# Optimization experiments

Measured on AMD Instinct MI355X. Metric: run time of the kernel, lower is better.

The kernel has to match this reference:

```python
import jax, jax.numpy as jnp
import numpy as np

N_U, N_M, E, L = 100000, 20000, 2000000, 500000
F_U, F_M, H = 64, 128, 128


def setup_inputs() -> dict:
    key = jax.random.key(0)
    ks = jax.random.split(key, 48)
    p = lambda k, shape: jax.random.normal(k, shape, jnp.float32) * 0.02
    inp = {
        'x_user': jax.random.normal(ks[0], (N_U, F_U), jnp.float32),
        'x_movie': jax.random.normal(ks[1], (N_M, F_M), jnp.float32),
        'edge_index': jnp.stack([jax.random.randint(ks[2], (E,), 0, N_U),
                                 jax.random.randint(ks[3], (E,), 0, N_M)]),
        'edge_label_index': jnp.stack([jax.random.randint(ks[4], (L,), 0, N_U),
                                       jax.random.randint(ks[5], (L,), 0, N_M)]),
        # per-type input projections (LazyLinear)
        'lin_u_W': p(ks[6], (H, F_U)), 'lin_u_b': p(ks[7], (H,)),
        'lin_m_W': p(ks[8], (H, F_M)), 'lin_m_b': p(ks[9], (H,)),
        # BatchNorm (eval mode: running stats)
        'bn_u_g': 1.0 + p(ks[10], (H,)), 'bn_u_b': p(ks[11], (H,)),
        'bn_u_m': p(ks[12], (H,)) * 5.0,
        'bn_u_v': jax.random.uniform(ks[13], (H,), jnp.float32, 0.5, 1.5),
        'bn_m_g': 1.0 + p(ks[14], (H,)), 'bn_m_b': p(ks[15], (H,)),
        'bn_m_m': p(ks[16], (H,)) * 5.0,
        'bn_m_v': jax.random.uniform(ks[17], (H,), jnp.float32, 0.5, 1.5),
        # conv1: SAGEConv per relation (Wl applied to aggregated, Wr to root)
        'c1_um_Wl': p(ks[18], (H, H)), 'c1_um_bl': p(ks[19], (H,)), 'c1_um_Wr': p(ks[20], (H, H)),
        'c1_mu_Wl': p(ks[21], (H, H)), 'c1_mu_bl': p(ks[22], (H,)), 'c1_mu_Wr': p(ks[23], (H, H)),
        # conv2
        'c2_um_Wl': p(ks[24], (H, H)), 'c2_um_bl': p(ks[25], (H,)), 'c2_um_Wr': p(ks[26], (H, H)),
        'c2_mu_Wl': p(ks[27], (H, H)), 'c2_mu_bl': p(ks[28], (H,)), 'c2_mu_Wr': p(ks[29], (H, H)),
        # edge decoder MLP: 2H -> 4H -> 2H -> 1
        'dec_W1': p(ks[30], (4 * H, 2 * H)), 'dec_b1': p(ks[31], (4 * H,)),
        'dec_W2': p(ks[32], (2 * H, 4 * H)), 'dec_b2': p(ks[33], (2 * H,)),
        'dec_W3': p(ks[34], (1, 2 * H)), 'dec_b3': p(ks[35], (1,)),
    }
    return inp


def _bn(x, g, b, m, v):
    return (x - m) * jax.lax.rsqrt(v + 1e-5) * g + b


def _seg_mean(msg, dst, n):
    s = jax.ops.segment_sum(msg, dst, num_segments=n)
    c = jax.ops.segment_sum(jnp.ones((dst.shape[0], 1), msg.dtype), dst, num_segments=n)
    return s / jnp.maximum(c, 1.0)


def _sage(x_src, x_dst, src, dst, Wl, bl, Wr):
    # PyG SAGEConv(aggr='mean'): lin_l(mean of source msgs) + lin_r(x_dst)
    agg = _seg_mean(x_src[src], dst, x_dst.shape[0])
    return agg @ Wl.T + bl + x_dst @ Wr.T


def reference(x_user, x_movie, edge_index, edge_label_index,
              lin_u_W, lin_u_b, lin_m_W, lin_m_b,
              bn_u_g, bn_u_b, bn_u_m, bn_u_v,
              bn_m_g, bn_m_b, bn_m_m, bn_m_v,
              c1_um_Wl, c1_um_bl, c1_um_Wr, c1_mu_Wl, c1_mu_bl, c1_mu_Wr,
              c2_um_Wl, c2_um_bl, c2_um_Wr, c2_mu_Wl, c2_mu_bl, c2_mu_Wr,
              dec_W1, dec_b1, dec_W2, dec_b2, dec_W3, dec_b3):
    u, m = edge_index[0], edge_index[1]
    # per-type projection + BN(eval) + ReLU (Dropout is identity in eval)
    xu = jnp.maximum(_bn(x_user @ lin_u_W.T + lin_u_b, bn_u_g, bn_u_b, bn_u_m, bn_u_v), 0.0)
    xm = jnp.maximum(_bn(x_movie @ lin_m_W.T + lin_m_b, bn_m_g, bn_m_b, bn_m_m, bn_m_v), 0.0)
    # conv1: user->movie and movie->user (HeteroConv mean over 1 relation each)
    xm1 = jnp.maximum(_sage(xu, xm, u, m, c1_um_Wl, c1_um_bl, c1_um_Wr), 0.0)
    xu1 = jnp.maximum(_sage(xm, xu, m, u, c1_mu_Wl, c1_mu_bl, c1_mu_Wr), 0.0)
    # conv2 (no activation after, matches forward)
    zm = _sage(xu1, xm1, u, m, c2_um_Wl, c2_um_bl, c2_um_Wr)
    zu = _sage(xm1, xu1, m, u, c2_mu_Wl, c2_mu_bl, c2_mu_Wr)
    # edge decoder: gather + MLP
    feat = jnp.concatenate([zu[edge_label_index[0]], zm[edge_label_index[1]]], axis=-1)
    h = jnp.maximum(feat @ dec_W1.T + dec_b1, 0.0)
    h = jnp.maximum(h @ dec_W2.T + dec_b2, 0.0)
    return (h @ dec_W3.T + dec_b3)[:, 0]
```

## Files before the change

### kernel.cpp

```cpp
#include <hip/hip_runtime.h>

#define NU 100000
#define NM 20000
#define NE 2000000
#define NL 500000
#define H  128
#define MROW 48

typedef __attribute__((ext_vector_type(8))) short bf16x8;
typedef __attribute__((ext_vector_type(4))) float floatx4;
typedef __attribute__((ext_vector_type(8))) unsigned short u16x8;
typedef __attribute__((ext_vector_type(4))) unsigned short u16x4;

__device__ __forceinline__ unsigned short f2b(float x) {
    union { __bf16 h; unsigned short u; } v;
    v.h = (__bf16)x;
    return v.u;
}
__device__ __forceinline__ float b2f(unsigned short h) {
    union { unsigned u; float f; } v; v.u = ((unsigned)h) << 16;
    return v.f;
}

#define SFCH(r, c)  ((r) * 32 + (((c) + (r)) & 31))
#define SH1CH(r, c) ((r) * 16 + (((c) + (r)) & 15))
#define SH2CH(r, c) ((r) * 64 + (((c) + (r)) & 63))

struct PrepArgs {
    const float* luW; float* wtu;
    const float* lmW; float* wtm;
    const float* W1; const float* W2;
    unsigned short* W1p; unsigned short* W2p;
    const float* sw[8]; unsigned short* wsg;
    const int* ei; int* rp_m; int* rp_u; int* pos_m; int* pos_u;
};

__global__ __launch_bounds__(256) void prep1(PrepArgs a) {
    const int b = blockIdx.x, tid = threadIdx.x;
    if (b < 64) {
        const int n = H * 64;
        for (int i = b * 256 + tid; i < n; i += 64 * 256) {
            int r = i >> 6, c = i & 63;
            a.wtu[c * H + r] = a.luW[i];
        }
    } else if (b < 128) {
        const int n = H * H;
        for (int i = (b - 64) * 256 + tid; i < n; i += 64 * 256) {
            int r = i >> 7, c = i & 127;
            a.wtm[c * H + r] = a.lmW[i];
        }
    } else if (b < 384) {
        const int n = 512 * 256;
        for (int i = (b - 128) * 256 + tid; i < n; i += 256 * 256) {
            int j = i & 7, lane = (i >> 3) & 63;
            int ln = lane & 15, lq = lane >> 4;
            int kg1 = (i >> 9) & 7,  t1 = i >> 12;
            a.W1p[i] = f2b(a.W1[(t1 * 16 + ln) * 256 + kg1 * 32 + lq * 8 + j]);
            int kg2 = (i >> 9) & 15, t2 = i >> 13;
            a.W2p[i] = f2b(a.W2[(t2 * 16 + ln) * 512 + kg2 * 32 + lq * 8 + j]);
        }
    } else if (b < 512) {
        const int n = 8 * 16384;
        for (int i = (b - 384) * 256 + tid; i < n; i += 128 * 256) {
            int j = i & 7, lane = (i >> 3) & 63;
            int kg = (i >> 9) & 3, t = (i >> 11) & 7, wsel = i >> 14;
            int ln = lane & 15, lq = lane >> 4;
            a.wsg[i] = f2b(a.sw[wsel][(t * 16 + ln) * H + kg * 32 + lq * 8 + j]);
        }
    } else {
        for (int i = (b - 512) * 256 + tid; i < NE; i += 2048 * 256) {
            int u = a.ei[i], m = a.ei[NE + i];
            a.pos_u[i] = atomicAdd(&a.rp_u[u + 1], 1);
            a.pos_m[i] = atomicAdd(&a.rp_m[m + 1], 1);
        }
    }
}

__global__ __launch_bounds__(256) void scan_p1(const int* __restrict__ rp_m, int n_m,
                                               const int* __restrict__ rp_u, int n_u,
                                               int* __restrict__ aux) {
    const int arr = blockIdx.y;
    const int* a = arr ? rp_u : rp_m;
    const int n  = arr ? n_u : n_m;
    const int nb = (n + 4095) >> 12;
    const int b  = blockIdx.x;
    if (b >= nb) return;
    __shared__ int s[256];
    const int tid = threadIdx.x;
    int i0 = (b << 12) + tid * 16;
    int run = 0;
#pragma unroll
    for (int i = 0; i < 16; ++i) { int idx = i0 + i; run += (idx < n) ? a[idx] : 0; }
    s[tid] = run;
    __syncthreads();
    for (int off = 128; off > 0; off >>= 1) {
        if (tid < off) s[tid] += s[tid + off];
        __syncthreads();
    }
    if (tid == 0) aux[arr * 32 + b] = s[0];
}

__global__ __launch_bounds__(256) void scan_p2(int* __restrict__ rp_m, int n_m,
                                               int* __restrict__ rp_u, int n_u,
                                               const int* __restrict__ aux) {
    const int arr = blockIdx.y;
    int* a = arr ? rp_u : rp_m;
    const int n  = arr ? n_u : n_m;
    const int nb = (n + 4095) >> 12;
    const int b  = blockIdx.x;
    if (b >= nb) return;
    __shared__ int s[256];
    __shared__ int sc;
    const int tid = threadIdx.x;
    if (tid == 0) {
        int c = 0;
        for (int i = 0; i < b; ++i) c += aux[arr * 32 + i];
        sc = c;
    }
    int i0 = (b << 12) + tid * 16;
    int v[16];
    int run = 0;
#pragma unroll
    for (int i = 0; i < 16; ++i) {
        int idx = i0 + i;
        int x = (idx < n) ? a[idx] : 0;
        run += x; v[i] = run;
    }
    s[tid] = run;
    __syncthreads();
    for (int off = 1; off < 256; off <<= 1) {
        int t = (tid >= off) ? s[tid - off] : 0;
        __syncthreads();
        s[tid] += t;
        __syncthreads();
    }
    int prev = sc + (tid > 0 ? s[tid - 1] : 0);
#pragma unroll
    for (int i = 0; i < 16; ++i) {
        int idx = i0 + i;
        if (idx < n) a[idx] = v[i] + prev;
    }
}

template <int K>
__device__ __forceinline__ void proj_body(
        const float* __restrict__ x, const float* __restrict__ Wt,
        const float* __restrict__ lb, const float* __restrict__ g,
        const float* __restrict__ bb, const float* __restrict__ bm,
        const float* __restrict__ bv, unsigned short* __restrict__ out, int N,
        int blk, float* sA) {
    const int tid = threadIdx.x;
    const int row0 = blk * 64;
    constexpr int F4 = K / 4;
#pragma unroll
    for (int i = 0; i < (64 * F4) / 256; ++i) {
        int idx = tid + i * 256;
        int r = idx / F4, c = idx - r * F4;
        int gr = min(row0 + r, N - 1);
        ((float4*)sA)[idx] = ((const float4*)(x + (size_t)gr * K))[c];
    }
    __syncthreads();
    const int h_t = tid & 31, r_t = tid >> 5;
    float acc[8][4] = {};
#pragma unroll 4
    for (int k = 0; k < K; k += 4) {
        float4 w[4];
#pragma unroll
        for (int kk = 0; kk < 4; ++kk)
            w[kk] = *(const float4*)(Wt + (k + kk) * H + h_t * 4);
#pragma unroll
        for (int rr = 0; rr < 8; ++rr) {
            float4 a = *(const float4*)(sA + (r_t * 8 + rr) * K + k);
            acc[rr][0] += a.x * w[0].x + a.y * w[1].x + a.z * w[2].x + a.w * w[3].x;
            acc[rr][1] += a.x * w[0].y + a.y * w[1].y + a.z * w[2].y + a.w * w[3].y;
            acc[rr][2] += a.x * w[0].z + a.y * w[1].z + a.z * w[2].z + a.w * w[3].z;
            acc[rr][3] += a.x * w[0].w + a.y * w[1].w + a.z * w[2].w + a.w * w[3].w;
        }
    }
    const int h = h_t * 4;
    float4 lb4 = *(const float4*)(lb + h);
    float4 g4  = *(const float4*)(g  + h);
    float4 bb4 = *(const float4*)(bb + h);
    float4 m4  = *(const float4*)(bm + h);
    float4 v4  = *(const float4*)(bv + h);
    float sc[4] = { g4.x * rsqrtf(v4.x + 1e-5f), g4.y * rsqrtf(v4.y + 1e-5f),
                    g4.z * rsqrtf(v4.z + 1e-5f), g4.w * rsqrtf(v4.w + 1e-5f) };
    float lbv[4] = { lb4.x, lb4.y, lb4.z, lb4.w };
    float mv[4]  = { m4.x, m4.y, m4.z, m4.w };
    float bbv[4] = { bb4.x, bb4.y, bb4.z, bb4.w };
#pragma unroll
    for (int rr = 0; rr < 8; ++rr) {
        int gr = row0 + r_t * 8 + rr;
        if (gr < N) {
            u16x4 o;
#pragma unroll
            for (int c = 0; c < 4; ++c)
                o[c] = f2b(fmaxf((acc[rr][c] + lbv[c] - mv[c]) * sc[c] + bbv[c], 0.0f));
            *(u16x4*)(out + (size_t)gr * H + h) = o;
        }
    }
}

struct PBArgs {
    const int* ei; const int* rp_m; const int* rp_u;
    const int* pos_m; const int* pos_u; int* es_m; int* es_u;
    const float* xu; const float* wtu;
    const float* lub; const float* bug; const float* bub; const float* bum; const float* buv;
    unsigned short* xu_b;
    const float* xm; const float* wtm;
    const float* lmb; const float* bmg; const float* bmb; const float* bmm; const float* bmv;
    unsigned short* xm_b;
    int nbu;
};

__global__ __launch_bounds__(256, 2) void projbucket(PBArgs a) {
    __shared__ float sA[64 * H];
    const int b = blockIdx.x;
    if (b < 2048) {
        for (int i = b * 256 + threadIdx.x; i < NE; i += 2048 * 256) {
            int u = a.ei[i], m = a.ei[NE + i];
            a.es_m[a.rp_m[m] + a.pos_m[i]] = u;
            a.es_u[a.rp_u[u] + a.pos_u[i]] = m;
        }
    } else if (b < 2048 + a.nbu) {
        proj_body<64>(a.xu, a.wtu, a.lub, a.bug, a.bub, a.bum, a.buv, a.xu_b, NU,
                      b - 2048, sA);
    } else {
        proj_body<128>(a.xm, a.wtm, a.lmb, a.bmg, a.bmb, a.bmm, a.bmv, a.xm_b, NM,
                       b - 2048 - a.nbu, sA);
    }
}

__global__ __launch_bounds__(256) void agg_bf16(
        const unsigned short* __restrict__ srcA, const int* __restrict__ esA,
        const int* __restrict__ rpA, unsigned short* __restrict__ outA, int nA,
        const unsigned short* __restrict__ srcB, const int* __restrict__ esB,
        const int* __restrict__ rpB, unsigned short* __restrict__ outB, int nB) {
    int wid = blockIdx.x * 4 + (threadIdx.x >> 6);
    const int lane = threadIdx.x & 63;
    const unsigned short* src; const int* es; const int* rp; unsigned short* out; int n;
    if (wid < nA) { src = srcA; es = esA; rp = rpA; out = outA; n = wid; }
    else {
        wid -= nA;
        if (wid >= nB) return;
        src = srcB; es = esB; rp = rpB; out = outB; n = wid;
    }
    const int start = rp[n], end = rp[n + 1];
    const int cb = (lane & 15) * 8;
    const int ro = lane >> 4;
    float acc[8] = {};
    if (end > start) {
        int j = start;
        for (; j + 16 <= end; j += 16) {
            u16x8 v0 = *(const u16x8*)(src + (size_t)es[j +      ro] * H + cb);
            u16x8 v1 = *(const u16x8*)(src + (size_t)es[j +  4 + ro] * H + cb);
            u16x8 v2 = *(const u16x8*)(src + (size_t)es[j +  8 + ro] * H + cb);
            u16x8 v3 = *(const u16x8*)(src + (size_t)es[j + 12 + ro] * H + cb);
#pragma unroll
            for (int e = 0; e < 8; ++e)
                acc[e] += b2f(v0[e]) + b2f(v1[e]) + b2f(v2[e]) + b2f(v3[e]);
        }
        for (; j + 4 <= end; j += 4) {
            u16x8 v = *(const u16x8*)(src + (size_t)es[j + ro] * H + cb);
#pragma unroll
            for (int e = 0; e < 8; ++e) acc[e] += b2f(v[e]);
        }
        if (j < end) {
            int idx = j + ro;
            int row = es[idx < end ? idx : end - 1];
            float m = (idx < end) ? 1.0f : 0.0f;
            u16x8 v = *(const u16x8*)(src + (size_t)row * H + cb);
#pragma unroll
            for (int e = 0; e < 8; ++e) acc[e] = fmaf(m, b2f(v[e]), acc[e]);
        }
    }
#pragma unroll
    for (int e = 0; e < 8; ++e) {
        acc[e] += __shfl_xor(acc[e], 16);
        acc[e] += __shfl_xor(acc[e], 32);
    }
    float inv = (end > start) ? 1.0f / (float)(end - start) : 0.0f;
    if (ro == 0) {
        u16x8 o;
#pragma unroll
        for (int e = 0; e < 8; ++e) o[e] = f2b(acc[e] * inv);
        *(u16x8*)(out + (size_t)n * H + cb) = o;
    }
}

__global__ __launch_bounds__(256, 4) void sage_mfma(
        const unsigned short* __restrict__ aggA, const unsigned short* __restrict__ xA,
        const unsigned short* __restrict__ WlA, const unsigned short* __restrict__ WrA,
        const float* __restrict__ blA, unsigned short* __restrict__ outA, int NA, int NBLKA,
        const unsigned short* __restrict__ aggB, const unsigned short* __restrict__ xB,
        const unsigned short* __restrict__ WlB, const unsigned short* __restrict__ WrB,
        const float* __restrict__ blB, unsigned short* __restrict__ outB, int NB,
        int relu) {
    __shared__ unsigned short sAg[64 * 16 * 8];
    __shared__ unsigned short sX[64 * 16 * 8];
    const int tid = threadIdx.x;
    const unsigned short *agg, *x, *Wl, *Wr; const float* bl; unsigned short* out;
    int N, row0;
    if ((int)blockIdx.x < NBLKA) {
        agg = aggA; x = xA; Wl = WlA; Wr = WrA; bl = blA; out = outA; N = NA;
        row0 = blockIdx.x * 64;
    } else {
        agg = aggB; x = xB; Wl = WlB; Wr = WrB; bl = blB; out = outB; N = NB;
        row0 = (blockIdx.x - NBLKA) * 64;
    }
#pragma unroll
    for (int i = 0; i < 4; ++i) {
        int idx = tid + i * 256;
        int r = idx >> 4, c = idx & 15;
        int gr = min(row0 + r, N - 1);
        *(u16x8*)(sAg + SH1CH(r, c) * 8) = *(const u16x8*)(agg + (size_t)gr * H + c * 8);
        *(u16x8*)(sX  + SH1CH(r, c) * 8) = *(const u16x8*)(x   + (size_t)gr * H + c * 8);
    }
    __syncthreads();
    const int lane = tid & 63, w = tid >> 6;
    const int ln = lane & 15, lq = lane >> 4;
    floatx4 acc[2][4] = {};
#pragma unroll 2
    for (int kg = 0; kg < 4; ++kg) {
        bf16x8 aA[4], aX[4];
#pragma unroll
        for (int mt = 0; mt < 4; ++mt) {
            aA[mt] = *(const bf16x8*)(sAg + SH1CH(mt * 16 + ln, kg * 4 + lq) * 8);
            aX[mt] = *(const bf16x8*)(sX  + SH1CH(mt * 16 + ln, kg * 4 + lq) * 8);
        }
#pragma unroll
        for (int nt = 0; nt < 2; ++nt) {
            int widx = ((w * 2 + nt) * 4 + kg) * 512 + lane * 8;
            bf16x8 bL = *(const bf16x8*)(Wl + widx);
            bf16x8 bR = *(const bf16x8*)(Wr + widx);
#pragma unroll
            for (int mt = 0; mt < 4; ++mt) {
                acc[nt][mt] = __builtin_amdgcn_mfma_f32_16x16x32_bf16(aA[mt], bL, acc[nt][mt], 0, 0, 0);
                acc[nt][mt] = __builtin_amdgcn_mfma_f32_16x16x32_bf16(aX[mt], bR, acc[nt][mt], 0, 0, 0);
            }
        }
    }
    __syncthreads();
    {
#pragma unroll
        for (int nt = 0; nt < 2; ++nt) {
            int ncol = w * 32 + nt * 16 + ln;
            float bv = bl[ncol];
            int cch = ncol >> 3, coff = ncol & 7;
#pragma unroll
            for (int mt = 0; mt < 4; ++mt)
#pragma unroll
                for (int i = 0; i < 4; ++i) {
                    int row = mt * 16 + lq * 4 + i;
                    float v = acc[nt][mt][i] + bv;
                    if (relu) v = fmaxf(v, 0.0f);
                    sAg[SH1CH(row, cch) * 8 + coff] = f2b(v);
                }
        }
    }
    __syncthreads();
#pragma unroll
    for (int i = 0; i < 4; ++i) {
        int idx = tid + i * 256;
        int r = idx >> 4, c = idx & 15;
        int gr = row0 + r;
        if (gr < N)
            *(u16x8*)(out + (size_t)gr * H + c * 8) = *(const u16x8*)(sAg + SH1CH(r, c) * 8);
    }
}

__global__ __launch_bounds__(512, 4) void decoder_mfma(
        const unsigned short* __restrict__ zu, const unsigned short* __restrict__ zm,
        const int* __restrict__ eli,
        const unsigned short* __restrict__ W1p, const float* __restrict__ b1,
        const unsigned short* __restrict__ W2p, const float* __restrict__ b2,
        const float* __restrict__ W3, const float* __restrict__ b3,
        float* __restrict__ out) {
    __shared__ unsigned short sF[MROW * 32 * 8];
    __shared__ unsigned short sH1[MROW * 64 * 8];
    const int tid = threadIdx.x;
    const int row0 = blockIdx.x * MROW;
    {
        int r = tid >> 3, p = tid & 7;
        if (r < MROW) {
            int rg = min(row0 + r, NL - 1);
            int iu = eli[rg], im = eli[NL + rg];
            const unsigned short* zur = zu + (size_t)iu * H;
            const unsigned short* zmr = zm + (size_t)im * H;
#pragma unroll
            for (int j = 0; j < 4; ++j) {
                int c = p + j * 8;
                const unsigned short* s = (c < 16) ? (zur + c * 8) : (zmr + (c - 16) * 8);
                *(u16x8*)(sF + SFCH(r, c) * 8) = *(const u16x8*)s;
            }
        }
    }
    __syncthreads();
    const int lane = tid & 63, w = tid >> 6;
    const int ln = lane & 15, lq = lane >> 4;
    {
        floatx4 acc1[4][3] = {};
        const unsigned short* w1base = W1p + ((size_t)(w * 4) * 8) * 512 + lane * 8;
#pragma unroll 2
        for (int kg = 0; kg < 8; ++kg) {
            bf16x8 fb[3];
#pragma unroll
            for (int mt = 0; mt < 3; ++mt)
                fb[mt] = *(const bf16x8*)(sF + SFCH(mt * 16 + ln, kg * 4 + lq) * 8);
#pragma unroll
            for (int nt = 0; nt < 4; ++nt) {
                bf16x8 wa = *(const bf16x8*)(w1base + (size_t)(nt * 8 + kg) * 512);
#pragma unroll
                for (int mt = 0; mt < 3; ++mt)
                    acc1[nt][mt] = __builtin_amdgcn_mfma_f32_16x16x32_bf16(wa, fb[mt], acc1[nt][mt], 0, 0, 0);
            }
        }
#pragma unroll
        for (int nt = 0; nt < 4; ++nt) {
            int colbase = w * 64 + nt * 16 + lq * 4;
            float4 bv = *(const float4*)(b1 + colbase);
            int cch = colbase >> 3, coff = colbase & 7;
#pragma unroll
            for (int mt = 0; mt < 3; ++mt) {
                int erow = mt * 16 + ln;
                u16x4 o = { f2b(fmaxf(acc1[nt][mt][0] + bv.x, 0.0f)),
                            f2b(fmaxf(acc1[nt][mt][1] + bv.y, 0.0f)),
                            f2b(fmaxf(acc1[nt][mt][2] + bv.z, 0.0f)),
                            f2b(fmaxf(acc1[nt][mt][3] + bv.w, 0.0f)) };
                *(u16x4*)(sH1 + SH2CH(erow, cch) * 8 + coff) = o;
            }
        }
    }
    __syncthreads();
    floatx4 acc3[2][3] = {};
    {
        const unsigned short* w2base = W2p + ((size_t)(w * 2) * 16) * 512 + lane * 8;
#pragma unroll 2
        for (int kg = 0; kg < 16; ++kg) {
            bf16x8 hb[3];
#pragma unroll
            for (int mt = 0; mt < 3; ++mt)
                hb[mt] = *(const bf16x8*)(sH1 + SH2CH(mt * 16 + ln, kg * 4 + lq) * 8);
#pragma unroll
            for (int nt = 0; nt < 2; ++nt) {
                bf16x8 wa = *(const bf16x8*)(w2base + (size_t)(nt * 16 + kg) * 512);
#pragma unroll
                for (int mt = 0; mt < 3; ++mt)
                    acc3[nt][mt] = __builtin_amdgcn_mfma_f32_16x16x32_bf16(wa, hb[mt], acc3[nt][mt], 0, 0, 0);
            }
        }
    }
    float* sP = (float*)sF;
    {
        float4 w3a = *(const float4*)(W3 + w * 32 + lq * 4);
        float4 w3b = *(const float4*)(W3 + w * 32 + 16 + lq * 4);
        float4 b2a = *(const float4*)(b2 + w * 32 + lq * 4);
        float4 b2b = *(const float4*)(b2 + w * 32 + 16 + lq * 4);
#pragma unroll
        for (int mt = 0; mt < 3; ++mt) {
            float s =
                fmaxf(acc3[0][mt][0] + b2a.x, 0.0f) * w3a.x +
                fmaxf(acc3[0][mt][1] + b2a.y, 0.0f) * w3a.y +
                fmaxf(acc3[0][mt][2] + b2a.z, 0.0f) * w3a.z +
                fmaxf(acc3[0][mt][3] + b2a.w, 0.0f) * w3a.w +
                fmaxf(acc3[1][mt][0] + b2b.x, 0.0f) * w3b.x +
                fmaxf(acc3[1][mt][1] + b2b.y, 0.0f) * w3b.y +
                fmaxf(acc3[1][mt][2] + b2b.z, 0.0f) * w3b.z +
                fmaxf(acc3[1][mt][3] + b2b.w, 0.0f) * w3b.w;
            sP[(mt * 16 + ln) * 36 + w * 4 + lq] = s;
        }
    }
    __syncthreads();
    {
        int r = tid >> 3, p = tid & 7;
        if (r < MROW) {
            float4 v = *(const float4*)(sP + r * 36 + p * 4);
            float sum = v.x + v.y + v.z + v.w;
            sum += __shfl_down(sum, 4, 8);
            sum += __shfl_down(sum, 2, 8);
            sum += __shfl_down(sum, 1, 8);
            if (p == 0 && row0 + r < NL) out[row0 + r] = sum + b3[0];
        }
    }
}

extern "C" void kernel_launch(void* const* d_in, const int* in_sizes, int n_in,
                              void* d_out, int out_size, void* d_ws, size_t ws_size,
                              hipStream_t stream) {
    const float* x_user  = (const float*)d_in[0];
    const float* x_movie = (const float*)d_in[1];
    const int*   ei      = (const int*)d_in[2];
    const int*   eli     = (const int*)d_in[3];
    const float* lin_u_W = (const float*)d_in[4];
    const float* lin_u_b = (const float*)d_in[5];
    const float* lin_m_W = (const float*)d_in[6];
    const float* lin_m_b = (const float*)d_in[7];
    const float* bn_u_g  = (const float*)d_in[8];
    const float* bn_u_b  = (const float*)d_in[9];
    const float* bn_u_m  = (const float*)d_in[10];
    const float* bn_u_v  = (const float*)d_in[11];
    const float* bn_m_g  = (const float*)d_in[12];
    const float* bn_m_b  = (const float*)d_in[13];
    const float* bn_m_m  = (const float*)d_in[14];
    const float* bn_m_v  = (const float*)d_in[15];
    const float* c1_um_Wl = (const float*)d_in[16];
    const float* c1_um_bl = (const float*)d_in[17];
    const float* c1_um_Wr = (const float*)d_in[18];
    const float* c1_mu_Wl = (const float*)d_in[19];
    const float* c1_mu_bl = (const float*)d_in[20];
    const float* c1_mu_Wr = (const float*)d_in[21];
    const float* c2_um_Wl = (const float*)d_in[22];
    const float* c2_um_bl = (const float*)d_in[23];
    const float* c2_um_Wr = (const float*)d_in[24];
    const float* c2_mu_Wl = (const float*)d_in[25];
    const float* c2_mu_bl = (const float*)d_in[26];
    const float* c2_mu_Wr = (const float*)d_in[27];
    const float* dec_W1 = (const float*)d_in[28];
    const float* dec_b1 = (const float*)d_in[29];
    const float* dec_W2 = (const float*)d_in[30];
    const float* dec_b2 = (const float*)d_in[31];
    const float* dec_W3 = (const float*)d_in[32];
    const float* dec_b3 = (const float*)d_in[33];

    char* base = (char*)d_ws;
    size_t off = 0;
    auto alloc = [&](size_t bytes) -> char* {
        char* p = base + off;
        off += (bytes + 255) & ~(size_t)255;
        return p;
    };
    unsigned short* xu_b  = (unsigned short*)alloc((size_t)NU * H * 2);
    unsigned short* xm_b  = (unsigned short*)alloc((size_t)NM * H * 2);
    unsigned short* xu1_b = (unsigned short*)alloc((size_t)NU * H * 2);
    unsigned short* xm1_b = (unsigned short*)alloc((size_t)NM * H * 2);
    unsigned short* aggu  = (unsigned short*)alloc((size_t)NU * H * 2);
    unsigned short* aggm  = (unsigned short*)alloc((size_t)NM * H * 2);
    float* wt_u = (float*)alloc((size_t)64 * H * 4);
    float* wt_m = (float*)alloc((size_t)H * H * 4);
    unsigned short* wsg = (unsigned short*)alloc((size_t)8 * 16384 * 2);
    unsigned short* w1p = (unsigned short*)alloc((size_t)512 * 256 * 2);
    unsigned short* w2p = (unsigned short*)alloc((size_t)256 * 512 * 2);
    int* rp_m  = (int*)alloc((size_t)(NM + 1) * 4);
    int* rp_u  = (int*)alloc((size_t)(NU + 1) * 4);
    int* es_m  = (int*)alloc((size_t)NE * 4);
    int* es_u  = (int*)alloc((size_t)NE * 4);
    int* scan_aux = (int*)alloc((size_t)64 * 4);
    unsigned short* zu = xu_b;
    unsigned short* zm = xm_b;
    int* pos_m = (int*)aggu;
    int* pos_u = pos_m + NE;

    hipMemsetAsync(rp_m, 0, (size_t)((char*)es_m - (char*)rp_m), stream);

    PrepArgs pa;
    pa.luW = lin_u_W; pa.wtu = wt_u;
    pa.lmW = lin_m_W; pa.wtm = wt_m;
    pa.W1 = dec_W1; pa.W2 = dec_W2; pa.W1p = w1p; pa.W2p = w2p;
    pa.sw[0] = c1_um_Wl; pa.sw[1] = c1_um_Wr; pa.sw[2] = c1_mu_Wl; pa.sw[3] = c1_mu_Wr;
    pa.sw[4] = c2_um_Wl; pa.sw[5] = c2_um_Wr; pa.sw[6] = c2_mu_Wl; pa.sw[7] = c2_mu_Wr;
    pa.wsg = wsg;
    pa.ei = ei; pa.rp_m = rp_m; pa.rp_u = rp_u; pa.pos_m = pos_m; pa.pos_u = pos_u;
    prep1<<<2560, 256, 0, stream>>>(pa);

    scan_p1<<<dim3(25, 2), 256, 0, stream>>>(rp_m, NM + 1, rp_u, NU + 1, scan_aux);
    scan_p2<<<dim3(25, 2), 256, 0, stream>>>(rp_m, NM + 1, rp_u, NU + 1, scan_aux);

    const int NBU = (NU + 63) / 64, NBM = (NM + 63) / 64;
    PBArgs pb;
    pb.ei = ei; pb.rp_m = rp_m; pb.rp_u = rp_u;
    pb.pos_m = pos_m; pb.pos_u = pos_u; pb.es_m = es_m; pb.es_u = es_u;
    pb.xu = x_user; pb.wtu = wt_u;
    pb.lub = lin_u_b; pb.bug = bn_u_g; pb.bub = bn_u_b; pb.bum = bn_u_m; pb.buv = bn_u_v;
    pb.xu_b = xu_b;
    pb.xm = x_movie; pb.wtm = wt_m;
    pb.lmb = lin_m_b; pb.bmg = bn_m_g; pb.bmb = bn_m_b; pb.bmm = bn_m_m; pb.bmv = bn_m_v;
    pb.xm_b = xm_b;
    pb.nbu = NBU;
    projbucket<<<2048 + NBU + NBM, 256, 0, stream>>>(pb);

    const unsigned short* W_c1um_l = wsg + 0 * 16384;
    const unsigned short* W_c1um_r = wsg + 1 * 16384;
    const unsigned short* W_c1mu_l = wsg + 2 * 16384;
    const unsigned short* W_c1mu_r = wsg + 3 * 16384;
    const unsigned short* W_c2um_l = wsg + 4 * 16384;
    const unsigned short* W_c2um_r = wsg + 5 * 16384;
    const unsigned short* W_c2mu_l = wsg + 6 * 16384;
    const unsigned short* W_c2mu_r = wsg + 7 * 16384;

    const int AGG_BLOCKS = (NM + NU + 3) / 4;
    const int NBLK_M = (NM + 63) / 64, NBLK_U = (NU + 63) / 64;

    agg_bf16<<<AGG_BLOCKS, 256, 0, stream>>>(xu_b, es_m, rp_m, aggm, NM,
                                             xm_b, es_u, rp_u, aggu, NU);
    sage_mfma<<<NBLK_M + NBLK_U, 256, 0, stream>>>(
        aggm, xm_b, W_c1um_l, W_c1um_r, c1_um_bl, xm1_b, NM, NBLK_M,
        aggu, xu_b, W_c1mu_l, W_c1mu_r, c1_mu_bl, xu1_b, NU, 1);
    agg_bf16<<<AGG_BLOCKS, 256, 0, stream>>>(xu1_b, es_m, rp_m, aggm, NM,
                                             xm1_b, es_u, rp_u, aggu, NU);
    sage_mfma<<<NBLK_M + NBLK_U, 256, 0, stream>>>(
        aggm, xm1_b, W_c2um_l, W_c2um_r, c2_um_bl, zm, NM, NBLK_M,
        aggu, xu1_b, W_c2mu_l, W_c2mu_r, c2_mu_bl, zu, NU, 0);

    decoder_mfma<<<(NL + MROW - 1) / MROW, 512, 0, stream>>>(
        zu, zm, eli, w1p, dec_b1, w2p, dec_b2, dec_W3, dec_b3, (float*)d_out);
}
```

Measured before the change: 948.0 us.

## Fuse neighbor mean aggregation into SAGE MFMA kernel via shared memory

Removes the separate aggregation kernel. Each SAGE block now gathers and averages its own 64 destination rows' neighbor features straight into shared memory before the MFMA stage. This drops the round trip of the aggregated tensors through global memory and two kernel launches. In exchange, each block works through 16 rows serially per wave, which lowers gather parallelism and latency hiding compared with one wave per node, and the pos buffers now need their own workspace allocation.

```diff
diff --git a/kernel.cpp b/kernel.cpp
--- a/kernel.cpp
+++ b/kernel.cpp
@@ -231,93 +231,84 @@
     }
 }
 
-__global__ __launch_bounds__(256) void agg_bf16(
-        const unsigned short* __restrict__ srcA, const int* __restrict__ esA,
-        const int* __restrict__ rpA, unsigned short* __restrict__ outA, int nA,
-        const unsigned short* __restrict__ srcB, const int* __restrict__ esB,
-        const int* __restrict__ rpB, unsigned short* __restrict__ outB, int nB) {
-    int wid = blockIdx.x * 4 + (threadIdx.x >> 6);
-    const int lane = threadIdx.x & 63;
-    const unsigned short* src; const int* es; const int* rp; unsigned short* out; int n;
-    if (wid < nA) { src = srcA; es = esA; rp = rpA; out = outA; n = wid; }
-    else {
-        wid -= nA;
-        if (wid >= nB) return;
-        src = srcB; es = esB; rp = rpB; out = outB; n = wid;
-    }
-    const int start = rp[n], end = rp[n + 1];
-    const int cb = (lane & 15) * 8;
-    const int ro = lane >> 4;
-    float acc[8] = {};
-    if (end > start) {
-        int j = start;
-        for (; j + 16 <= end; j += 16) {
-            u16x8 v0 = *(const u16x8*)(src + (size_t)es[j +      ro] * H + cb);
-            u16x8 v1 = *(const u16x8*)(src + (size_t)es[j +  4 + ro] * H + cb);
-            u16x8 v2 = *(const u16x8*)(src + (size_t)es[j +  8 + ro] * H + cb);
-            u16x8 v3 = *(const u16x8*)(src + (size_t)es[j + 12 + ro] * H + cb);
-#pragma unroll
-            for (int e = 0; e < 8; ++e)
-                acc[e] += b2f(v0[e]) + b2f(v1[e]) + b2f(v2[e]) + b2f(v3[e]);
-        }
-        for (; j + 4 <= end; j += 4) {
-            u16x8 v = *(const u16x8*)(src + (size_t)es[j + ro] * H + cb);
-#pragma unroll
-            for (int e = 0; e < 8; ++e) acc[e] += b2f(v[e]);
-        }
-        if (j < end) {
-            int idx = j + ro;
-            int row = es[idx < end ? idx : end - 1];
-            float m = (idx < end) ? 1.0f : 0.0f;
-            u16x8 v = *(const u16x8*)(src + (size_t)row * H + cb);
-#pragma unroll
-            for (int e = 0; e < 8; ++e) acc[e] = fmaf(m, b2f(v[e]), acc[e]);
-        }
-    }
-#pragma unroll
-    for (int e = 0; e < 8; ++e) {
-        acc[e] += __shfl_xor(acc[e], 16);
-        acc[e] += __shfl_xor(acc[e], 32);
-    }
-    float inv = (end > start) ? 1.0f / (float)(end - start) : 0.0f;
-    if (ro == 0) {
-        u16x8 o;
-#pragma unroll
-        for (int e = 0; e < 8; ++e) o[e] = f2b(acc[e] * inv);
-        *(u16x8*)(out + (size_t)n * H + cb) = o;
-    }
-}
-
-__global__ __launch_bounds__(256, 4) void sage_mfma(
-        const unsigned short* __restrict__ aggA, const unsigned short* __restrict__ xA,
+__global__ __launch_bounds__(256, 4) void sage_agg_mfma(
+        const unsigned short* __restrict__ gsrcA, const int* __restrict__ esA,
+        const int* __restrict__ rpA, const unsigned short* __restrict__ xA,
         const unsigned short* __restrict__ WlA, const unsigned short* __restrict__ WrA,
         const float* __restrict__ blA, unsigned short* __restrict__ outA, int NA, int NBLKA,
-        const unsigned short* __restrict__ aggB, const unsigned short* __restrict__ xB,
+        const unsigned short* __restrict__ gsrcB, const int* __restrict__ esB,
+        const int* __restrict__ rpB, const unsigned short* __restrict__ xB,
         const unsigned short* __restrict__ WlB, const unsigned short* __restrict__ WrB,
         const float* __restrict__ blB, unsigned short* __restrict__ outB, int NB,
         int relu) {
     __shared__ unsigned short sAg[64 * 16 * 8];
     __shared__ unsigned short sX[64 * 16 * 8];
     const int tid = threadIdx.x;
-    const unsigned short *agg, *x, *Wl, *Wr; const float* bl; unsigned short* out;
-    int N, row0;
+    const unsigned short *gsrc, *x, *Wl, *Wr; const int *es, *rp; const float* bl;
+    unsigned short* out; int N, row0;
     if ((int)blockIdx.x < NBLKA) {
-        agg = aggA; x = xA; Wl = WlA; Wr = WrA; bl = blA; out = outA; N = NA;
-        row0 = blockIdx.x * 64;
+        gsrc = gsrcA; es = esA; rp = rpA; x = xA; Wl = WlA; Wr = WrA; bl = blA;
+        out = outA; N = NA; row0 = blockIdx.x * 64;
     } else {
-        agg = aggB; x = xB; Wl = WlB; Wr = WrB; bl = blB; out = outB; N = NB;
-        row0 = (blockIdx.x - NBLKA) * 64;
+        gsrc = gsrcB; es = esB; rp = rpB; x = xB; Wl = WlB; Wr = WrB; bl = blB;
+        out = outB; N = NB; row0 = (blockIdx.x - NBLKA) * 64;
     }
 #pragma unroll
     for (int i = 0; i < 4; ++i) {
         int idx = tid + i * 256;
         int r = idx >> 4, c = idx & 15;
         int gr = min(row0 + r, N - 1);
-        *(u16x8*)(sAg + SH1CH(r, c) * 8) = *(const u16x8*)(agg + (size_t)gr * H + c * 8);
-        *(u16x8*)(sX  + SH1CH(r, c) * 8) = *(const u16x8*)(x   + (size_t)gr * H + c * 8);
-    }
-    __syncthreads();
+        *(u16x8*)(sX + SH1CH(r, c) * 8) = *(const u16x8*)(x + (size_t)gr * H + c * 8);
+    }
     const int lane = tid & 63, w = tid >> 6;
+    {
+        const int cb = (lane & 15) * 8;
+        const int ro = lane >> 4;
+        for (int k = 0; k < 16; ++k) {
+            int r = w * 16 + k;
+            int node = min(row0 + r, N - 1);
+            const int start = rp[node], end = rp[node + 1];
+            float acc[8] = {};
+            if (end > start) {
+                int j = start;
+                for (; j + 16 <= end; j += 16) {
+                    u16x8 v0 = *(const u16x8*)(gsrc + (size_t)es[j +      ro] * H + cb);
+                    u16x8 v1 = *(const u16x8*)(gsrc + (size_t)es[j +  4 + ro] * H + cb);
+                    u16x8 v2 = *(const u16x8*)(gsrc + (size_t)es[j +  8 + ro] * H + cb);
+                    u16x8 v3 = *(const u16x8*)(gsrc + (size_t)es[j + 12 + ro] * H + cb);
+#pragma unroll
+                    for (int e = 0; e < 8; ++e)
+                        acc[e] += b2f(v0[e]) + b2f(v1[e]) + b2f(v2[e]) + b2f(v3[e]);
+                }
+                for (; j + 4 <= end; j += 4) {
+                    u16x8 v = *(const u16x8*)(gsrc + (size_t)es[j + ro] * H + cb);
+#pragma unroll
+                    for (int e = 0; e < 8; ++e) acc[e] += b2f(v[e]);
+                }
+                if (j < end) {
+                    int idx = j + ro;
+                    int row = es[idx < end ? idx : end - 1];
+                    float m = (idx < end) ? 1.0f : 0.0f;
+                    u16x8 v = *(const u16x8*)(gsrc + (size_t)row * H + cb);
+#pragma unroll
+                    for (int e = 0; e < 8; ++e) acc[e] = fmaf(m, b2f(v[e]), acc[e]);
+                }
+            }
+#pragma unroll
+            for (int e = 0; e < 8; ++e) {
+                acc[e] += __shfl_xor(acc[e], 16);
+                acc[e] += __shfl_xor(acc[e], 32);
+            }
+            float inv = (end > start) ? 1.0f / (float)(end - start) : 0.0f;
+            if (ro == 0) {
+                u16x8 o;
+#pragma unroll
+                for (int e = 0; e < 8; ++e) o[e] = f2b(acc[e] * inv);
+                *(u16x8*)(sAg + SH1CH(r, lane & 15) * 8) = o;
+            }
+        }
+    }
+    __syncthreads();
     const int ln = lane & 15, lq = lane >> 4;
     floatx4 acc[2][4] = {};
 #pragma unroll 2
@@ -533,8 +524,6 @@
     unsigned short* xm_b  = (unsigned short*)alloc((size_t)NM * H * 2);
     unsigned short* xu1_b = (unsigned short*)alloc((size_t)NU * H * 2);
     unsigned short* xm1_b = (unsigned short*)alloc((size_t)NM * H * 2);
-    unsigned short* aggu  = (unsigned short*)alloc((size_t)NU * H * 2);
-    unsigned short* aggm  = (unsigned short*)alloc((size_t)NM * H * 2);
     float* wt_u = (float*)alloc((size_t)64 * H * 4);
     float* wt_m = (float*)alloc((size_t)H * H * 4);
     unsigned short* wsg = (unsigned short*)alloc((size_t)8 * 16384 * 2);
@@ -544,11 +533,11 @@
     int* rp_u  = (int*)alloc((size_t)(NU + 1) * 4);
     int* es_m  = (int*)alloc((size_t)NE * 4);
     int* es_u  = (int*)alloc((size_t)NE * 4);
+    int* pos_m = (int*)alloc((size_t)NE * 4);
+    int* pos_u = (int*)alloc((size_t)NE * 4);
     int* scan_aux = (int*)alloc((size_t)64 * 4);
     unsigned short* zu = xu_b;
     unsigned short* zm = xm_b;
-    int* pos_m = (int*)aggu;
-    int* pos_u = pos_m + NE;
 
     hipMemsetAsync(rp_m, 0, (size_t)((char*)es_m - (char*)rp_m), stream);
 
@@ -587,19 +576,14 @@
     const unsigned short* W_c2mu_l = wsg + 6 * 16384;
     const unsigned short* W_c2mu_r = wsg + 7 * 16384;
 
-    const int AGG_BLOCKS = (NM + NU + 3) / 4;
     const int NBLK_M = (NM + 63) / 64, NBLK_U = (NU + 63) / 64;
 
-    agg_bf16<<<AGG_BLOCKS, 256, 0, stream>>>(xu_b, es_m, rp_m, aggm, NM,
-                                             xm_b, es_u, rp_u, aggu, NU);
-    sage_mfma<<<NBLK_M + NBLK_U, 256, 0, stream>>>(
-        aggm, xm_b, W_c1um_l, W_c1um_r, c1_um_bl, xm1_b, NM, NBLK_M,
-        aggu, xu_b, W_c1mu_l, W_c1mu_r, c1_mu_bl, xu1_b, NU, 1);
-    agg_bf16<<<AGG_BLOCKS, 256, 0, stream>>>(xu1_b, es_m, rp_m, aggm, NM,
-                                             xm1_b, es_u, rp_u, aggu, NU);
-    sage_mfma<<<NBLK_M + NBLK_U, 256, 0, stream>>>(
-        aggm, xm1_b, W_c2um_l, W_c2um_r, c2_um_bl, zm, NM, NBLK_M,
-        aggu, xu1_b, W_c2mu_l, W_c2mu_r, c2_mu_bl, zu, NU, 0);
+    sage_agg_mfma<<<NBLK_M + NBLK_U, 256, 0, stream>>>(
+        xu_b, es_m, rp_m, xm_b, W_c1um_l, W_c1um_r, c1_um_bl, xm1_b, NM, NBLK_M,
+        xm_b, es_u, rp_u, xu_b, W_c1mu_l, W_c1mu_r, c1_mu_bl, xu1_b, NU, 1);
+    sage_agg_mfma<<<NBLK_M + NBLK_U, 256, 0, stream>>>(
+        xu1_b, es_m, rp_m, xm1_b, W_c2um_l, W_c2um_r, c2_um_bl, zm, NM, NBLK_M,
+        xm1_b, es_u, rp_u, xu1_b, W_c2mu_l, W_c2mu_r, c2_mu_bl, zu, NU, 0);
 
     decoder_mfma<<<(NL + MROW - 1) / MROW, 512, 0, stream>>>(
         zu, zm, eli, w1p, dec_b1, w2p, dec_b2, dec_W3, dec_b3, (float*)d_out);
```

Measured after the change: 1.021 ms. 1.08x slower.
